# Optimization experiments

Measured on AMD Instinct MI355X. Metric: run time of the kernel, lower is better.

## Reference

```python
import jax, jax.numpy as jnp
import numpy as np

B, N, D = 64, 128, 32
P = N * (N - 1)          # ordered pairs
H1, H2, HF = 32, 32, 16  # layer_widths=(32,32), final_widths=(16,)
EPS = 1e-5
SLOPE = 0.01             # LeakyReLU default


def _leaky(x):
    return jnp.where(x >= 0, x, SLOPE * x)


def setup_inputs() -> dict:
    key = jax.random.key(0)
    ks = jax.random.split(key, 16)
    # all ordered pairs (i, j), i != j, grouped by source i
    src = np.repeat(np.arange(N), N - 1)
    tgt = np.array([j for i in range(N) for j in range(N) if j != i])
    s = 0.1
    return {
        "inputs": jax.random.normal(ks[0], (B, N, D), jnp.float32),
        "src": jnp.asarray(src, jnp.int32),
        "tgt": jnp.asarray(tgt, jnp.int32),
        # edge MLP: Linear(2D,32) -> BN1d(P) -> LeakyReLU -> Linear(32,32) -> LeakyReLU -> Linear(32, 1+D)
        "W1": jax.random.normal(ks[1], (2 * D, H1), jnp.float32) * s,
        "b1": jnp.zeros((H1,), jnp.float32),
        "g1": jnp.ones((P,), jnp.float32),
        "be1": jnp.zeros((P,), jnp.float32),
        "W2": jax.random.normal(ks[2], (H1, H2), jnp.float32) * s,
        "b2": jnp.zeros((H2,), jnp.float32),
        "W3": jax.random.normal(ks[3], (H2, 1 + D), jnp.float32) * s,
        "b3": jnp.zeros((1 + D,), jnp.float32),
        # final MLP: Linear(2D,16) -> BN1d(16) -> LeakyReLU -> Linear(16, D)
        "Wf1": jax.random.normal(ks[4], (2 * D, HF), jnp.float32) * s,
        "bf1": jnp.zeros((HF,), jnp.float32),
        "gf": jnp.ones((HF,), jnp.float32),
        "bef": jnp.zeros((HF,), jnp.float32),
        "Wf2": jax.random.normal(ks[5], (HF, D), jnp.float32) * s,
        "bf2": jnp.zeros((D,), jnp.float32),
    }


def reference(inputs, src, tgt, W1, b1, g1, be1, W2, b2, W3, b3,
              Wf1, bf1, gf, bef, Wf2, bf2):
    b, n, d = inputs.shape
    # gather pair features: (B, P, 2D)
    paired = jnp.concatenate([inputs[:, src], inputs[:, tgt]], axis=2)
    h = paired @ W1 + b1                              # (B, P, H1)
    # BatchNorm1d(P) on (B, P, H1): normalize per pair channel over (batch, feat)
    m = h.mean(axis=(0, 2), keepdims=True)
    v = h.var(axis=(0, 2), keepdims=True)
    h = (h - m) * jax.lax.rsqrt(v + EPS) * g1[None, :, None] + be1[None, :, None]
    h = _leaky(h) @ W2 + b2
    h = _leaky(h) @ W3 + b3                           # (B, P, 1+D)
    edges = jax.nn.sigmoid(h[..., :1])                # (B, P, 1)
    messages = h[..., 1:]                             # (B, P, D)
    weighted = edges * messages
    # segment-sum over the (N-1) senders per source node
    agg = weighted.reshape(b, n, n - 1, d).sum(axis=2)  # (B, N, D)
    sm = jnp.concatenate([inputs, agg], axis=2).reshape(-1, 2 * d)
    f = sm @ Wf1 + bf1                                # (B*N, HF)
    mf = f.mean(axis=0)
    vf = f.var(axis=0)
    f = (f - mf) * jax.lax.rsqrt(vf + EPS) * gf + bef
    out = _leaky(f) @ Wf2 + bf2
    return edges[..., 0], out.reshape(b, n, d)
```

## Files before the change

kernel.cpp:

```cpp
#include <hip/hip_runtime.h>
#include <hip/hip_bf16.h>
#include <math.h>

#define BB 64
#define NN 128
#define DD 32
#define PP (NN * (NN - 1))
#define EPSF 1e-5f

typedef __attribute__((ext_vector_type(8))) short bf16x8;
typedef __attribute__((ext_vector_type(4))) float f32x4;
typedef __attribute__((ext_vector_type(2))) float f32x2;

static __device__ __forceinline__ unsigned pk2bf(float a, float b) {
    float2 t; t.x = a; t.y = b;
    __hip_bfloat162 h = __float22bfloat162_rn(t);
    unsigned u;
    __builtin_memcpy(&u, &h, 4);
    return u;
}
static __device__ __forceinline__ unsigned short f2bf(float x) {
    return (unsigned short)pk2bf(x, x);
}
static __device__ __forceinline__ float leakyf(float x) {
    return fmaxf(x, 0.01f * x);
}

__global__ __launch_bounds__(256) void proj_kernel(
    const float* __restrict__ inputs, const float* __restrict__ W1,
    const float* __restrict__ b1,
    const float* __restrict__ W2, const float* __restrict__ W3,
    float* __restrict__ AT, float* __restrict__ BT,
    unsigned short* __restrict__ ATh, unsigned short* __restrict__ BTh,
    float* __restrict__ SQp,
    unsigned short* __restrict__ W2p, unsigned short* __restrict__ W3p,
    float* __restrict__ fpartA, float* __restrict__ fpartB)
{
    __shared__ float Xs[16 * 33];
    __shared__ float W1s[2048];
    __shared__ float red[16];

    int tid = threadIdx.x;
    int n = blockIdx.x >> 2, q = blockIdx.x & 3;

    for (int idx = tid; idx < 2048; idx += 256) W1s[idx] = W1[idx];
    for (int idx = tid; idx < 512; idx += 256) {
        int r = idx >> 5, d = idx & 31;
        Xs[r * 33 + d] = inputs[(q * 16 + r) * 4096 + n * 32 + d];
    }
    __syncthreads();

    int j = tid & 31, rb = tid >> 5;
    int lane = tid & 63, w = tid >> 6;
    float b1j = b1[j];
    float sa = 0.f, qa = 0.f, sb = 0.f, qb = 0.f;
    #pragma unroll
    for (int i = 0; i < 2; ++i) {
        int r = rb * 2 + i;
        int b = q * 16 + r;
        float a = b1j, c = 0.f;
        #pragma unroll
        for (int k = 0; k < 32; ++k) {
            float x = Xs[r * 33 + k];
            a += x * W1s[k * 32 + j];
            c += x * W1s[(32 + k) * 32 + j];
        }
        int off = (n * 64 + b) * 32 + j;
        AT[off] = a;  BT[off] = c;
        ATh[off] = f2bf(a);  BTh[off] = f2bf(c);
        sa += a; qa += a * a; sb += c; qb += c * c;
    }
    #pragma unroll
    for (int d = 32; d > 0; d >>= 1) {
        sa += __shfl_down(sa, d, 64);
        qa += __shfl_down(qa, d, 64);
        sb += __shfl_down(sb, d, 64);
        qb += __shfl_down(qb, d, 64);
    }
    if (lane == 0) { red[w*4+0] = sa; red[w*4+1] = qa; red[w*4+2] = sb; red[w*4+3] = qb; }
    __syncthreads();
    if (tid == 0) {
        float4 v;
        v.x = red[0] + red[4] + red[8]  + red[12];
        v.y = red[1] + red[5] + red[9]  + red[13];
        v.z = red[2] + red[6] + red[10] + red[14];
        v.w = red[3] + red[7] + red[11] + red[15];
        ((float4*)SQp)[n * 4 + q] = v;
    }

    if (blockIdx.x == 0 && tid < 64) {
        int l = tid, nn2 = l & 15, kc = l >> 4;
        #pragma unroll
        for (int ct = 0; ct < 2; ++ct)
            #pragma unroll
            for (int jj = 0; jj < 8; ++jj) {
                int k = kc * 8 + jj;
                W2p[(ct * 64 + l) * 8 + jj] = f2bf(W2[k * 32 + ct * 16 + nn2]);
            }
        #pragma unroll
        for (int ct = 0; ct < 3; ++ct)
            #pragma unroll
            for (int jj = 0; jj < 8; ++jj) {
                int k = kc * 8 + jj;
                int c2 = ct * 16 + nn2;
                W3p[(ct * 64 + l) * 8 + jj] = f2bf(c2 < 33 ? W3[k * 33 + c2] : 0.f);
            }
    }
    if (blockIdx.x == 1) {
        for (int idx = tid; idx < 1024; idx += 256) {
            fpartA[idx] = 0.f;
            fpartB[idx] = 0.f;
        }
    }
}

__global__ __launch_bounds__(256) void stats2_kernel(
    const unsigned short* __restrict__ ATh, const unsigned short* __restrict__ BTh,
    const float* __restrict__ SQp,
    const float* __restrict__ g1, const float* __restrict__ be1,
    float* __restrict__ statAB)
{
    __shared__ __align__(16) float part[4 * 64 * 4];
    int tid = threadIdx.x;
    int lane = tid & 63, w = tid >> 6;
    int s0 = (blockIdx.x >> 3) * 16, t0 = (blockIdx.x & 7) * 16;

    int m = lane & 15, kc = lane >> 4;
    const unsigned short* abase = ATh + (s0 + m) * 2048 + kc * 8 + w * 512;
    const unsigned short* bbase = BTh + (t0 + m) * 2048 + kc * 8 + w * 512;

    f32x4 acc0 = {0.f, 0.f, 0.f, 0.f}, acc1 = {0.f, 0.f, 0.f, 0.f};
    #pragma unroll
    for (int step = 0; step < 8; ++step) {
        bf16x8 av0 = *(const bf16x8*)(abase + (2 * step) * 32);
        bf16x8 bv0 = *(const bf16x8*)(bbase + (2 * step) * 32);
        acc0 = __builtin_amdgcn_mfma_f32_16x16x32_bf16(av0, bv0, acc0, 0, 0, 0);
        bf16x8 av1 = *(const bf16x8*)(abase + (2 * step + 1) * 32);
        bf16x8 bv1 = *(const bf16x8*)(bbase + (2 * step + 1) * 32);
        acc1 = __builtin_amdgcn_mfma_f32_16x16x32_bf16(av1, bv1, acc1, 0, 0, 0);
    }
    f32x4 acc;
    acc[0] = acc0[0] + acc1[0]; acc[1] = acc0[1] + acc1[1];
    acc[2] = acc0[2] + acc1[2]; acc[3] = acc0[3] + acc1[3];
    *(f32x4*)&part[(w * 64 + lane) * 4] = acc;
    __syncthreads();

    if (w == 0) {
        #pragma unroll
        for (int ww = 1; ww < 4; ++ww) {
            f32x4 o2 = *(const f32x4*)&part[(ww * 64 + lane) * 4];
            acc[0] += o2[0]; acc[1] += o2[1]; acc[2] += o2[2]; acc[3] += o2[3];
        }
        int col = lane & 15, quad = lane >> 4;
        int t = t0 + col;
        float sbt = 0.f, qbt = 0.f;
        #pragma unroll
        for (int o2 = 0; o2 < 4; ++o2) {
            float4 v = ((const float4*)SQp)[t * 4 + o2];
            sbt += v.z; qbt += v.w;
        }
        #pragma unroll
        for (int r = 0; r < 4; ++r) {
            int s = s0 + quad * 4 + r;
            if (s != t) {
                float sas = 0.f, qas = 0.f;
                #pragma unroll
                for (int o2 = 0; o2 < 4; ++o2) {
                    float4 v = ((const float4*)SQp)[s * 4 + o2];
                    sas += v.x; qas += v.y;
                }
                int e = t - (t > s);
                int p = s * 127 + e;
                float S = sas + sbt;
                float Q = qas + qbt + 2.f * acc[r];
                float mean = S * (1.f / 2048.f);
                float var  = Q * (1.f / 2048.f) - mean * mean;
                float inv  = rsqrtf(var + EPSF);
                float sc   = inv * g1[p];
                float2 o;
                o.x = sc;
                o.y = be1[p] - mean * sc;
                ((float2*)statAB)[p] = o;
            }
        }
    }
}

__global__ __launch_bounds__(256, 8) void edges_kernel(
    const float* __restrict__ AT, const float* __restrict__ BT,
    const float* __restrict__ statAB,
    const unsigned short* __restrict__ W2p, const unsigned short* __restrict__ W3p,
    const float* __restrict__ b2, const float* __restrict__ b3,
    const float* __restrict__ inputs, const float* __restrict__ Wf1,
    const float* __restrict__ bf1,
    float* __restrict__ edges_out,
    float* __restrict__ f, float* __restrict__ fpartA, float* __restrict__ fpartB)
{
    __shared__ __align__(16) unsigned short Hs[4][512];
    __shared__ float Wf1s[1024];
    __shared__ float aggbuf[4][32];

    int tid = threadIdx.x;
    int s = blockIdx.x & 127;
    int b = blockIdx.x >> 7;
    int lane = tid & 63, w = tid >> 6;
    int m = lane & 15;
    int kb = lane >> 4;
    int col = m;
    int q4 = kb * 4;
    int qbase = lane & 48;

    for (int idx = tid; idx < 1024; idx += 256) Wf1s[idx] = Wf1[idx];

    bf16x8 wb2[2], wb3[3];
    wb2[0] = *(const bf16x8*)(W2p + (0 * 64 + lane) * 8);
    wb2[1] = *(const bf16x8*)(W2p + (1 * 64 + lane) * 8);
    wb3[0] = *(const bf16x8*)(W3p + (0 * 64 + lane) * 8);
    wb3[1] = *(const bf16x8*)(W3p + (1 * 64 + lane) * 8);
    wb3[2] = *(const bf16x8*)(W3p + (2 * 64 + lane) * 8);
    float b2c0 = b2[col], b2c1 = b2[16 + col];
    float b3c[3];
    #pragma unroll
    for (int ct = 0; ct < 3; ++ct) {
        int c = ct * 16 + col;
        b3c[ct] = (c < 33) ? b3[c] : 0.f;
    }

    const float4* asl = (const float4*)(AT + (s * 64 + b) * 32 + kb * 8);
    float4 a0 = asl[0], a1 = asl[1];
    f32x2 av[4];
    av[0][0]=a0.x; av[0][1]=a0.y; av[1][0]=a0.z; av[1][1]=a0.w;
    av[2][0]=a1.x; av[2][1]=a1.y; av[3][0]=a1.z; av[3][1]=a1.w;

    float aggpart[3] = {0.f, 0.f, 0.f};

    #pragma unroll
    for (int rt = 0; rt < 2; ++rt) {
        int tile = w * 2 + rt;
        int e = tile * 16 + m;
        bool valid = (e < 127);
        int ee = valid ? e : 0;
        int t = ee + (ee >= s);
        int p = s * 127 + ee;
        float2 st = ((const float2*)statAB)[p];
        float sc = valid ? st.x : 0.f;
        float sh = valid ? st.y : 0.f;
        f32x2 sc2; sc2[0] = sc; sc2[1] = sc;
        f32x2 sh2; sh2[0] = sh; sh2[1] = sh;

        const float4* bsl = (const float4*)(BT + (t * 64 + b) * 32 + kb * 8);
        float4 bv0 = bsl[0], bv1 = bsl[1];
        f32x2 bv[4];
        bv[0][0]=bv0.x; bv[0][1]=bv0.y; bv[1][0]=bv0.z; bv[1][1]=bv0.w;
        bv[2][0]=bv1.x; bv[2][1]=bv1.y; bv[3][0]=bv1.z; bv[3][1]=bv1.w;

        union { bf16x8 v; unsigned u[4]; } AF;
        #pragma unroll
        for (int i = 0; i < 4; ++i) {
            f32x2 y = (av[i] + bv[i]) * sc2 + sh2;
            f32x2 tq = y * 0.01f;
            float n0 = fmaxf(y[0], tq[0]);
            float n1 = fmaxf(y[1], tq[1]);
            AF.u[i] = pk2bf(n0, n1);
        }

        f32x4 c0 = {0.f, 0.f, 0.f, 0.f}, c1 = {0.f, 0.f, 0.f, 0.f};
        c0 = __builtin_amdgcn_mfma_f32_16x16x32_bf16(AF.v, wb2[0], c0, 0, 0, 0);
        c1 = __builtin_amdgcn_mfma_f32_16x16x32_bf16(AF.v, wb2[1], c1, 0, 0, 0);

        #pragma unroll
        for (int reg = 0; reg < 4; ++reg) {
            int row = q4 + reg;
            float x = leakyf(c0[reg] + b2c0);
            float y = leakyf(c1[reg] + b2c1);
            int cA = col;
            int cB = col + 16;
            Hs[w][row * 32 + (((cA >> 3) ^ (row >> 2)) & 3) * 8 + (cA & 7)] = f2bf(x);
            Hs[w][row * 32 + (((cB >> 3) ^ (row >> 2)) & 3) * 8 + (cB & 7)] = f2bf(y);
        }
        bf16x8 a2 = *(const bf16x8*)&Hs[w][m * 32 + ((kb ^ (m >> 2)) & 3) * 8];

        f32x4 oo[3];
        #pragma unroll
        for (int ct = 0; ct < 3; ++ct) {
            f32x4 cc = {0.f, 0.f, 0.f, 0.f};
            oo[ct] = __builtin_amdgcn_mfma_f32_16x16x32_bf16(a2, wb3[ct], cc, 0, 0, 0);
        }

        float v0 = 0.f, v1 = 0.f, v2 = 0.f, v3 = 0.f;
        int grow0 = tile * 16 + q4;
        if (col == 0) {
            v0 = 1.f / (1.f + __expf(-(oo[0][0] + b3c[0])));
            v1 = 1.f / (1.f + __expf(-(oo[0][1] + b3c[0])));
            v2 = 1.f / (1.f + __expf(-(oo[0][2] + b3c[0])));
            v3 = (grow0 == 124) ? 0.f
               : 1.f / (1.f + __expf(-(oo[0][3] + b3c[0])));
            float* ep = edges_out + b * PP + s * 127 + grow0;
            ep[0] = v0; ep[1] = v1; ep[2] = v2;
            if (grow0 != 124) ep[3] = v3;
        }
        float ev0 = __shfl(v0, qbase, 64);
        float ev1 = __shfl(v1, qbase, 64);
        float ev2 = __shfl(v2, qbase, 64);
        float ev3 = __shfl(v3, qbase, 64);

        #pragma unroll
        for (int ct = 0; ct < 3; ++ct) {
            float bb3 = b3c[ct];
            float pt = ev0 * (oo[ct][0] + bb3) + ev1 * (oo[ct][1] + bb3)
                     + ev2 * (oo[ct][2] + bb3) + ev3 * (oo[ct][3] + bb3);
            aggpart[ct] += pt;
        }
    }

    #pragma unroll
    for (int ct = 0; ct < 3; ++ct) {
        float pt = aggpart[ct];
        pt += __shfl_xor(pt, 16, 64);
        pt += __shfl_xor(pt, 32, 64);
        int c = ct * 16 + col;
        if (kb == 0 && c >= 1 && c <= 32) aggbuf[w][c - 1] = pt;
    }
    __syncthreads();

    if (w == 0) {
        int j = lane & 15, kg = lane >> 4;
        int row = b * 128 + s;
        const float* xrow = inputs + row * 32;
        float acc = 0.f;
        if (kg < 2) {
            #pragma unroll
            for (int i = 0; i < 16; ++i) {
                int k = kg * 16 + i;
                acc += xrow[k] * Wf1s[k * 16 + j];
            }
        } else {
            #pragma unroll
            for (int i = 0; i < 16; ++i) {
                int k = (kg - 2) * 16 + i;
                float tot = aggbuf[0][k] + aggbuf[1][k] + aggbuf[2][k] + aggbuf[3][k];
                acc += tot * Wf1s[(32 + k) * 16 + j];
            }
        }
        acc += __shfl_xor(acc, 16, 64);
        acc += __shfl_xor(acc, 32, 64);
        if (lane < 16) {
            acc += bf1[j];
            f[row * 16 + j] = acc;
            int bucket = blockIdx.x & 63;
            atomicAdd(&fpartA[bucket * 16 + j], acc);
            atomicAdd(&fpartB[bucket * 16 + j], acc * acc);
        }
    }
}

__global__ __launch_bounds__(256) void out_kernel(
    const float* __restrict__ f,
    const float* __restrict__ fpartA, const float* __restrict__ fpartB,
    const float* __restrict__ gf, const float* __restrict__ bef,
    const float* __restrict__ Wf2, const float* __restrict__ bf2,
    float* __restrict__ outp)
{
    __shared__ float Wf2s[512];
    __shared__ float sc[16], sh[16];
    __shared__ float fs[128];

    int tid = threadIdx.x;
    for (int idx = tid; idx < 512; idx += 256) Wf2s[idx] = Wf2[idx];
    if (tid < 16) {
        float S = 0.f, Q = 0.f;
        #pragma unroll
        for (int g = 0; g < 64; ++g) {
            S += fpartA[g * 16 + tid];
            Q += fpartB[g * 16 + tid];
        }
        float mean = S * (1.f / 8192.f);
        float var  = Q * (1.f / 8192.f) - mean * mean;
        float inv  = rsqrtf(var + EPSF);
        float s2   = inv * gf[tid];
        sc[tid] = s2;
        sh[tid] = bef[tid] - mean * s2;
    }
    int row0 = blockIdx.x * 8;
    if (tid < 128) {
        int r = tid >> 4, j = tid & 15;
        fs[r * 16 + j] = f[(row0 + r) * 16 + j];
    }
    __syncthreads();

    int rl = tid >> 5, d = tid & 31;
    float acc = bf2[d];
    #pragma unroll
    for (int j = 0; j < 16; ++j) {
        float v = fs[rl * 16 + j] * sc[j] + sh[j];
        v = leakyf(v);
        acc += v * Wf2s[j * 32 + d];
    }
    outp[(row0 + rl) * 32 + d] = acc;
}

extern "C" void kernel_launch(void* const* d_in, const int* in_sizes, int n_in,
                              void* d_out, int out_size, void* d_ws, size_t ws_size,
                              hipStream_t stream) {
    const float* inputs = (const float*)d_in[0];
    const float* W1   = (const float*)d_in[3];
    const float* b1   = (const float*)d_in[4];
    const float* g1   = (const float*)d_in[5];
    const float* be1  = (const float*)d_in[6];
    const float* W2   = (const float*)d_in[7];
    const float* b2   = (const float*)d_in[8];
    const float* W3   = (const float*)d_in[9];
    const float* b3   = (const float*)d_in[10];
    const float* Wf1  = (const float*)d_in[11];
    const float* bf1  = (const float*)d_in[12];
    const float* gf   = (const float*)d_in[13];
    const float* bef  = (const float*)d_in[14];
    const float* Wf2  = (const float*)d_in[15];
    const float* bf2  = (const float*)d_in[16];

    float* ws = (float*)d_ws;
    float* AT     = ws;
    float* BT     = ws + 262144;
    unsigned short* ATh = (unsigned short*)(ws + 524288);
    unsigned short* BTh = ATh + 262144;
    float* SQp    = ws + 786432;
    float* statAB = ws + 790528;
    float* f      = ws + 823040;
    float* fpartA = ws + 954112;
    float* fpartB = ws + 955136;
    unsigned short* W2p = (unsigned short*)(ws + 956160);
    unsigned short* W3p = W2p + 1024;

    float* edges_out = (float*)d_out;
    float* outp      = edges_out + (size_t)BB * PP;

    proj_kernel<<<512, 256, 0, stream>>>(inputs, W1, b1, W2, W3,
                                         AT, BT, ATh, BTh, SQp,
                                         W2p, W3p, fpartA, fpartB);
    stats2_kernel<<<64, 256, 0, stream>>>(ATh, BTh, SQp, g1, be1, statAB);
    edges_kernel<<<8192, 256, 0, stream>>>(AT, BT, statAB, W2p, W3p,
                                           b2, b3, inputs, Wf1, bf1,
                                           edges_out, f, fpartA, fpartB);
    out_kernel<<<1024, 256, 0, stream>>>(f, fpartA, fpartB, gf, bef, Wf2, bf2, outp);
}
```

Measured before the change: 146.2 us.

## Process two batches per edges block and stage edge outputs in shared memory

Each edges_kernel block now handles two batch indices for the same source node, which halves the grid and reuses the per-block Wf1 staging, weight fragments, and BN stat loads across both batches. Edge sigmoid values go to a shared buffer and are written out as coalesced rows after the barrier, replacing strided per-lane stores and the shuffles that broadcast them. The H tile switches from an XOR swizzle to a padded stride-40 layout. Register pressure rises, so the occupancy hint drops from 8 to 4 waves per SIMD, and fewer blocks may reduce latency hiding.

Result: faster. 138.5 us (-5.3%).

```diff
diff --git a/kernel.cpp b/kernel.cpp
--- a/kernel.cpp
+++ b/kernel.cpp
@@ -186,7 +186,7 @@
     }
 }
 
-__global__ __launch_bounds__(256, 8) void edges_kernel(
+__global__ __launch_bounds__(256, 4) void edges_kernel(
     const float* __restrict__ AT, const float* __restrict__ BT,
     const float* __restrict__ statAB,
     const unsigned short* __restrict__ W2p, const unsigned short* __restrict__ W3p,
@@ -196,19 +196,19 @@
     float* __restrict__ edges_out,
     float* __restrict__ f, float* __restrict__ fpartA, float* __restrict__ fpartB)
 {
-    __shared__ __align__(16) unsigned short Hs[4][512];
+    __shared__ __align__(16) unsigned short Hs[4][16 * 40];
     __shared__ float Wf1s[1024];
-    __shared__ float aggbuf[4][32];
+    __shared__ float aggbuf[2][4][32];
+    __shared__ __align__(16) float edgebuf[2][128];
 
     int tid = threadIdx.x;
-    int s = blockIdx.x & 127;
-    int b = blockIdx.x >> 7;
+    int s  = blockIdx.x & 127;
+    int b0 = (blockIdx.x >> 7) * 2;
     int lane = tid & 63, w = tid >> 6;
     int m = lane & 15;
     int kb = lane >> 4;
     int col = m;
     int q4 = kb * 4;
-    int qbase = lane & 48;
 
     for (int idx = tid; idx < 1024; idx += 256) Wf1s[idx] = Wf1[idx];
 
@@ -226,13 +226,16 @@
         b3c[ct] = (c < 33) ? b3[c] : 0.f;
     }
 
-    const float4* asl = (const float4*)(AT + (s * 64 + b) * 32 + kb * 8);
-    float4 a0 = asl[0], a1 = asl[1];
-    f32x2 av[4];
-    av[0][0]=a0.x; av[0][1]=a0.y; av[1][0]=a0.z; av[1][1]=a0.w;
-    av[2][0]=a1.x; av[2][1]=a1.y; av[3][0]=a1.z; av[3][1]=a1.w;
-
-    float aggpart[3] = {0.f, 0.f, 0.f};
+    f32x2 av[2][4];
+    #pragma unroll
+    for (int bi = 0; bi < 2; ++bi) {
+        const float4* asl = (const float4*)(AT + (s * 64 + b0 + bi) * 32 + kb * 8);
+        float4 a0 = asl[0], a1 = asl[1];
+        av[bi][0][0]=a0.x; av[bi][0][1]=a0.y; av[bi][1][0]=a0.z; av[bi][1][1]=a0.w;
+        av[bi][2][0]=a1.x; av[bi][2][1]=a1.y; av[bi][3][0]=a1.z; av[bi][3][1]=a1.w;
+    }
+
+    float aggpart[2][3] = {{0.f,0.f,0.f},{0.f,0.f,0.f}};
 
     #pragma unroll
     for (int rt = 0; rt < 2; ++rt) {
@@ -241,91 +244,94 @@
         bool valid = (e < 127);
         int ee = valid ? e : 0;
         int t = ee + (ee >= s);
-        int p = s * 127 + ee;
-        float2 st = ((const float2*)statAB)[p];
+        float2 st = ((const float2*)statAB)[s * 127 + ee];
         float sc = valid ? st.x : 0.f;
         float sh = valid ? st.y : 0.f;
         f32x2 sc2; sc2[0] = sc; sc2[1] = sc;
         f32x2 sh2; sh2[0] = sh; sh2[1] = sh;
-
-        const float4* bsl = (const float4*)(BT + (t * 64 + b) * 32 + kb * 8);
-        float4 bv0 = bsl[0], bv1 = bsl[1];
-        f32x2 bv[4];
-        bv[0][0]=bv0.x; bv[0][1]=bv0.y; bv[1][0]=bv0.z; bv[1][1]=bv0.w;
-        bv[2][0]=bv1.x; bv[2][1]=bv1.y; bv[3][0]=bv1.z; bv[3][1]=bv1.w;
-
-        union { bf16x8 v; unsigned u[4]; } AF;
-        #pragma unroll
-        for (int i = 0; i < 4; ++i) {
-            f32x2 y = (av[i] + bv[i]) * sc2 + sh2;
-            f32x2 tq = y * 0.01f;
-            float n0 = fmaxf(y[0], tq[0]);
-            float n1 = fmaxf(y[1], tq[1]);
-            AF.u[i] = pk2bf(n0, n1);
-        }
-
-        f32x4 c0 = {0.f, 0.f, 0.f, 0.f}, c1 = {0.f, 0.f, 0.f, 0.f};
-        c0 = __builtin_amdgcn_mfma_f32_16x16x32_bf16(AF.v, wb2[0], c0, 0, 0, 0);
-        c1 = __builtin_amdgcn_mfma_f32_16x16x32_bf16(AF.v, wb2[1], c1, 0, 0, 0);
-
-        #pragma unroll
-        for (int reg = 0; reg < 4; ++reg) {
-            int row = q4 + reg;
-            float x = leakyf(c0[reg] + b2c0);
-            float y = leakyf(c1[reg] + b2c1);
-            int cA = col;
-            int cB = col + 16;
-            Hs[w][row * 32 + (((cA >> 3) ^ (row >> 2)) & 3) * 8 + (cA & 7)] = f2bf(x);
-            Hs[w][row * 32 + (((cB >> 3) ^ (row >> 2)) & 3) * 8 + (cB & 7)] = f2bf(y);
-        }
-        bf16x8 a2 = *(const bf16x8*)&Hs[w][m * 32 + ((kb ^ (m >> 2)) & 3) * 8];
-
-        f32x4 oo[3];
+        int grow0 = tile * 16 + q4;
+
+        #pragma unroll
+        for (int bi = 0; bi < 2; ++bi) {
+            const float4* bsl = (const float4*)(BT + (t * 64 + b0 + bi) * 32 + kb * 8);
+            float4 bv0 = bsl[0], bv1 = bsl[1];
+            f32x2 bv[4];
+            bv[0][0]=bv0.x; bv[0][1]=bv0.y; bv[1][0]=bv0.z; bv[1][1]=bv0.w;
+            bv[2][0]=bv1.x; bv[2][1]=bv1.y; bv[3][0]=bv1.z; bv[3][1]=bv1.w;
+
+            union { bf16x8 v; unsigned u[4]; } AF;
+            #pragma unroll
+            for (int i = 0; i < 4; ++i) {
+                f32x2 y = (av[bi][i] + bv[i]) * sc2 + sh2;
+                f32x2 tq = y * 0.01f;
+                float n0 = fmaxf(y[0], tq[0]);
+                float n1 = fmaxf(y[1], tq[1]);
+                AF.u[i] = pk2bf(n0, n1);
+            }
+
+            f32x4 c0 = {0.f, 0.f, 0.f, 0.f}, c1 = {0.f, 0.f, 0.f, 0.f};
+            c0 = __builtin_amdgcn_mfma_f32_16x16x32_bf16(AF.v, wb2[0], c0, 0, 0, 0);
+            c1 = __builtin_amdgcn_mfma_f32_16x16x32_bf16(AF.v, wb2[1], c1, 0, 0, 0);
+
+            #pragma unroll
+            for (int reg = 0; reg < 4; ++reg) {
+                int row = q4 + reg;
+                float x = leakyf(c0[reg] + b2c0);
+                float y = leakyf(c1[reg] + b2c1);
+                Hs[w][row * 40 + col]      = f2bf(x);
+                Hs[w][row * 40 + col + 16] = f2bf(y);
+            }
+            bf16x8 a2 = *(const bf16x8*)&Hs[w][m * 40 + kb * 8];
+
+            f32x4 oo[3];
+            #pragma unroll
+            for (int ct = 0; ct < 3; ++ct) {
+                f32x4 cc = {0.f, 0.f, 0.f, 0.f};
+                oo[ct] = __builtin_amdgcn_mfma_f32_16x16x32_bf16(a2, wb3[ct], cc, 0, 0, 0);
+            }
+
+            if (col == 0) {
+                float4 vv;
+                vv.x = 1.f / (1.f + __expf(-(oo[0][0] + b3c[0])));
+                vv.y = 1.f / (1.f + __expf(-(oo[0][1] + b3c[0])));
+                vv.z = 1.f / (1.f + __expf(-(oo[0][2] + b3c[0])));
+                vv.w = (grow0 == 124) ? 0.f
+                     : 1.f / (1.f + __expf(-(oo[0][3] + b3c[0])));
+                *(float4*)&edgebuf[bi][grow0] = vv;
+            }
+            f32x4 ev = *(const f32x4*)&edgebuf[bi][grow0];
+
+            #pragma unroll
+            for (int ct = 0; ct < 3; ++ct) {
+                float bb3 = b3c[ct];
+                float pt = ev[0] * (oo[ct][0] + bb3) + ev[1] * (oo[ct][1] + bb3)
+                         + ev[2] * (oo[ct][2] + bb3) + ev[3] * (oo[ct][3] + bb3);
+                aggpart[bi][ct] += pt;
+            }
+        }
+    }
+
+    #pragma unroll
+    for (int bi = 0; bi < 2; ++bi)
         #pragma unroll
         for (int ct = 0; ct < 3; ++ct) {
-            f32x4 cc = {0.f, 0.f, 0.f, 0.f};
-            oo[ct] = __builtin_amdgcn_mfma_f32_16x16x32_bf16(a2, wb3[ct], cc, 0, 0, 0);
-        }
-
-        float v0 = 0.f, v1 = 0.f, v2 = 0.f, v3 = 0.f;
-        int grow0 = tile * 16 + q4;
-        if (col == 0) {
-            v0 = 1.f / (1.f + __expf(-(oo[0][0] + b3c[0])));
-            v1 = 1.f / (1.f + __expf(-(oo[0][1] + b3c[0])));
-            v2 = 1.f / (1.f + __expf(-(oo[0][2] + b3c[0])));
-            v3 = (grow0 == 124) ? 0.f
-               : 1.f / (1.f + __expf(-(oo[0][3] + b3c[0])));
-            float* ep = edges_out + b * PP + s * 127 + grow0;
-            ep[0] = v0; ep[1] = v1; ep[2] = v2;
-            if (grow0 != 124) ep[3] = v3;
-        }
-        float ev0 = __shfl(v0, qbase, 64);
-        float ev1 = __shfl(v1, qbase, 64);
-        float ev2 = __shfl(v2, qbase, 64);
-        float ev3 = __shfl(v3, qbase, 64);
-
-        #pragma unroll
-        for (int ct = 0; ct < 3; ++ct) {
-            float bb3 = b3c[ct];
-            float pt = ev0 * (oo[ct][0] + bb3) + ev1 * (oo[ct][1] + bb3)
-                     + ev2 * (oo[ct][2] + bb3) + ev3 * (oo[ct][3] + bb3);
-            aggpart[ct] += pt;
-        }
-    }
-
-    #pragma unroll
-    for (int ct = 0; ct < 3; ++ct) {
-        float pt = aggpart[ct];
-        pt += __shfl_xor(pt, 16, 64);
-        pt += __shfl_xor(pt, 32, 64);
-        int c = ct * 16 + col;
-        if (kb == 0 && c >= 1 && c <= 32) aggbuf[w][c - 1] = pt;
-    }
+            float pt = aggpart[bi][ct];
+            pt += __shfl_xor(pt, 16, 64);
+            pt += __shfl_xor(pt, 32, 64);
+            int c = ct * 16 + col;
+            if (kb == 0 && c >= 1 && c <= 32) aggbuf[bi][w][c - 1] = pt;
+        }
     __syncthreads();
 
-    if (w == 0) {
+    if (tid < 127)
+        edges_out[b0 * PP + s * 127 + tid] = edgebuf[0][tid];
+    else if (tid >= 128 && tid < 255)
+        edges_out[(b0 + 1) * PP + s * 127 + (tid - 128)] = edgebuf[1][tid - 128];
+
+    if (w < 2) {
+        int bi = w;
         int j = lane & 15, kg = lane >> 4;
-        int row = b * 128 + s;
+        int row = (b0 + bi) * 128 + s;
         const float* xrow = inputs + row * 32;
         float acc = 0.f;
         if (kg < 2) {
@@ -338,7 +344,8 @@
             #pragma unroll
             for (int i = 0; i < 16; ++i) {
                 int k = (kg - 2) * 16 + i;
-                float tot = aggbuf[0][k] + aggbuf[1][k] + aggbuf[2][k] + aggbuf[3][k];
+                float tot = aggbuf[bi][0][k] + aggbuf[bi][1][k]
+                          + aggbuf[bi][2][k] + aggbuf[bi][3][k];
                 acc += tot * Wf1s[(32 + k) * 16 + j];
             }
         }
@@ -347,7 +354,7 @@
         if (lane < 16) {
             acc += bf1[j];
             f[row * 16 + j] = acc;
-            int bucket = blockIdx.x & 63;
+            int bucket = (blockIdx.x * 2 + bi) & 63;
             atomicAdd(&fpartA[bucket * 16 + j], acc);
             atomicAdd(&fpartB[bucket * 16 + j], acc * acc);
         }
@@ -438,7 +445,7 @@
                                          AT, BT, ATh, BTh, SQp,
                                          W2p, W3p, fpartA, fpartB);
     stats2_kernel<<<64, 256, 0, stream>>>(ATh, BTh, SQp, g1, be1, statAB);
-    edges_kernel<<<8192, 256, 0, stream>>>(AT, BT, statAB, W2p, W3p,
+    edges_kernel<<<4096, 256, 0, stream>>>(AT, BT, statAB, W2p, W3p,
                                            b2, b3, inputs, Wf1, bf1,
                                            edges_out, f, fpartA, fpartB);
     out_kernel<<<1024, 256, 0, stream>>>(f, fpartA, fpartB, gf, bef, Wf2, bf2, outp);
```
